# Optimization experiments

Hardware: AMD Instinct MI355X
Metric: run time of the kernel (lower is better)

The kernel has to match this reference:

```python
import jax, jax.numpy as jnp
import numpy as np

VOCAB = 50000
EMB = 128
HID = 256
H = HID // 2          # per-direction LSTM hidden
L = 59                # labelset size
B = 512
S = 256
START, STOP, PAD_LBL = 57, 58, 0
NEG = -10000.0


def setup_inputs() -> dict:
    key = jax.random.key(0)
    ks = jax.random.split(key, 12)
    inp = {}
    inp["x"] = jax.random.randint(ks[0], (B, S), 0, VOCAB)
    inp["y"] = jax.random.randint(ks[1], (B, S), 1, START)  # real labels only
    emb = jax.random.normal(ks[2], (VOCAB, EMB), jnp.float32) * 0.02
    inp["embed"] = emb.at[0].set(0.0)  # padding_idx=0

    def lstm_p(k):
        k1, k2, k3, k4 = jax.random.split(k, 4)
        s = 1.0 / np.sqrt(H)
        return (jax.random.uniform(k1, (4 * H, EMB), jnp.float32, -s, s),
                jax.random.uniform(k2, (4 * H, H), jnp.float32, -s, s),
                jax.random.uniform(k3, (4 * H,), jnp.float32, -s, s),
                jax.random.uniform(k4, (4 * H,), jnp.float32, -s, s))

    inp["Wih_f"], inp["Whh_f"], inp["bih_f"], inp["bhh_f"] = lstm_p(ks[3])
    inp["Wih_b"], inp["Whh_b"], inp["bih_b"], inp["bhh_b"] = lstm_p(ks[4])
    s = 1.0 / np.sqrt(HID)
    inp["Wout"] = jax.random.uniform(ks[5], (L, HID), jnp.float32, -s, s)
    inp["bout"] = jax.random.uniform(ks[6], (L,), jnp.float32, -s, s)
    T = jax.random.normal(ks[7], (L, L), jnp.float32)
    T = T.at[START, :].set(NEG)
    T = T.at[:, STOP].set(NEG)
    T = T.at[START, PAD_LBL].set(NEG)
    T = T.at[STOP + 1:, PAD_LBL].set(NEG)  # no-op here (STOP+1==L), kept for fidelity
    inp["trans"] = T
    inp["h0"] = jax.random.normal(ks[8], (2, B, H), jnp.float32)
    inp["c0"] = jax.random.normal(ks[9], (2, B, H), jnp.float32)
    return inp


def _lstm_scan(emb_seq, Wih, Whh, bih, bhh, h0, c0):
    # emb_seq: (S, B, E); PyTorch gate order i, f, g, o
    def step(carry, x_t):
        h, c = carry
        g = x_t @ Wih.T + bih + h @ Whh.T + bhh          # (B, 4H)
        i, f, gg, o = jnp.split(g, 4, axis=-1)
        c = jax.nn.sigmoid(f) * c + jax.nn.sigmoid(i) * jnp.tanh(gg)
        h = jax.nn.sigmoid(o) * jnp.tanh(c)
        return (h, c), h
    _, hs = jax.lax.scan(step, (h0, c0), emb_seq)
    return hs  # (S, B, H)


def reference(x, y, embed, Wih_f, Whh_f, bih_f, bhh_f,
              Wih_b, Whh_b, bih_b, bhh_b, Wout, bout, trans, h0, c0):
    # ---- BiLSTM emissions ----
    emb = embed[x]                                   # (B, S, E)
    emb = jnp.transpose(emb, (1, 0, 2))              # (S, B, E)
    hf = _lstm_scan(emb, Wih_f, Whh_f, bih_f, bhh_f, h0[0], c0[0])
    hb = _lstm_scan(emb[::-1], Wih_b, Whh_b, bih_b, bhh_b, h0[1], c0[1])[::-1]
    out = jnp.concatenate([hf, hb], axis=-1)         # (S, B, HID)
    feats = jnp.einsum('sbh,lh->bsl', out, Wout) + bout   # (B, S, L)

    # ---- CRF forward algorithm (log-sum-exp scan over time) ----
    alpha0 = jnp.full((B, L), NEG, feats.dtype).at[:, START].set(0.0)
    feats_t = jnp.transpose(feats, (1, 0, 2))        # (S, B, L)

    def fstep(alpha, f_t):
        # alpha_new[b, j] = f_t[b, j] + logsumexp_i(alpha[b, i] + trans[j, i])
        a = jax.nn.logsumexp(alpha[:, None, :] + trans[None, :, :], axis=2)
        return f_t + a, None

    alpha, _ = jax.lax.scan(fstep, alpha0, feats_t)
    fwd_score = jax.nn.logsumexp(alpha + trans[STOP][None, :], axis=1)  # (B,)

    # ---- gold path score ----
    yprev = jnp.concatenate([jnp.full((B, 1), START, y.dtype), y[:, :-1]], axis=1)
    emit = jnp.take_along_axis(feats, y[..., None], axis=2)[..., 0]     # (B, S)
    tr = trans[y, yprev]                                                # (B, S)
    gold = emit.sum(axis=1) + tr.sum(axis=1) + trans[STOP, y[:, -1]]

    return jnp.sum(fwd_score - gold)
```

## Files before the change

### kernel.cpp

```cpp
#include <hip/hip_runtime.h>

#define BB   512
#define SS   256
#define EE   128
#define HH   128
#define LL   59
#define STARTL 57
#define STOPL  58
#define VOCAB 50000

typedef float  f32x4  __attribute__((ext_vector_type(4)));
typedef short  bf16x8 __attribute__((ext_vector_type(8)));
typedef short  s16x4  __attribute__((ext_vector_type(4)));

__device__ __forceinline__ short f2bf(float f) {
    unsigned u = __float_as_uint(f);
    u += 0x7FFFu + ((u >> 16) & 1u);
    return (short)(u >> 16);
}
__device__ __forceinline__ float bf2f(unsigned short s) {
    return __uint_as_float(((unsigned)s) << 16);
}
__device__ __forceinline__ float sigf(float x) {
    float e = __builtin_amdgcn_exp2f(-1.44269504f * x);
    return __builtin_amdgcn_rcpf(1.0f + e);
}
__device__ __forceinline__ float tanhf_(float x) {
    float e = __builtin_amdgcn_exp2f(2.88539008f * x);
    return 1.0f - 2.0f * __builtin_amdgcn_rcpf(e + 1.0f);
}
__device__ __forceinline__ float wmax64(float v) {
    #pragma unroll
    for (int o = 32; o; o >>= 1) v = fmaxf(v, __shfl_xor(v, o));
    return v;
}
__device__ __forceinline__ float wsum64(float v) {
    #pragma unroll
    for (int o = 32; o; o >>= 1) v += __shfl_xor(v, o);
    return v;
}
__device__ __forceinline__ float rlane(float v, int i) {
    return __uint_as_float(__builtin_amdgcn_readlane(__float_as_uint(v), i));
}
__device__ __forceinline__ void bar_lds() {
    asm volatile("s_waitcnt lgkmcnt(0)\n\ts_barrier" ::: "memory");
}

__global__ __launch_bounds__(256) void conv_k(
    const float* __restrict__ embed,
    const float* __restrict__ Wih_f, const float* __restrict__ Wih_b,
    const float* __restrict__ Whh_f, const float* __restrict__ Whh_b,
    const float* __restrict__ bih_f, const float* __restrict__ bhh_f,
    const float* __restrict__ bih_b, const float* __restrict__ bhh_b,
    unsigned short* __restrict__ ebf, unsigned short* __restrict__ wix,
    unsigned short* __restrict__ whb, float* __restrict__ bsum)
{
    const int W1 = VOCAB * EE / 4;
    const int W2 = W1 + 2 * 16384;
    const int W3 = W2 + 2 * 16384;
    const int W4 = W3 + 1024;
    for (int i = blockIdx.x * blockDim.x + threadIdx.x; i < W4;
         i += gridDim.x * blockDim.x) {
        if (i < W1) {
            float4 v = ((const float4*)embed)[i];
            s16x4 s = { f2bf(v.x), f2bf(v.y), f2bf(v.z), f2bf(v.w) };
            ((s16x4*)ebf)[i] = s;
        } else if (i < W2) {
            const int j = i - W1, d = j >> 14, e = j & 16383;
            float4 v = ((const float4*)(d ? Wih_b : Wih_f))[e];
            s16x4 s = { f2bf(v.x), f2bf(v.y), f2bf(v.z), f2bf(v.w) };
            ((s16x4*)wix)[d * 16384 + e] = s;
        } else if (i < W3) {
            const int j = i - W2, d = j >> 14, e = j & 16383;
            float4 v = ((const float4*)(d ? Whh_b : Whh_f))[e];
            s16x4 s = { f2bf(v.x), f2bf(v.y), f2bf(v.z), f2bf(v.w) };
            ((s16x4*)whb)[d * 16384 + e] = s;
        } else {
            const int m = i - W3, d = m >> 9, c = m & 511;
            bsum[d * 512 + c] = d ? (bih_b[c] + bhh_b[c]) : (bih_f[c] + bhh_f[c]);
        }
    }
}

__global__ __launch_bounds__(512, 2) void lstm_f(
    const int* __restrict__ x, const unsigned short* __restrict__ ebf,
    const unsigned short* __restrict__ wix, const unsigned short* __restrict__ whb,
    const float* __restrict__ bsum,
    const float* __restrict__ h0, const float* __restrict__ c0,
    const float* __restrict__ Wout,
    unsigned short* __restrict__ fpF, unsigned short* __restrict__ fpB)
{
    const int tid = threadIdx.x;
    const int w = tid >> 6, l = tid & 63, qd = l >> 4, n = l & 15;
    const int rt = blockIdx.x & 127, dir = blockIdx.x >> 7;
    const int b0 = rt * 4;
    unsigned short* fp = dir ? fpB : fpF;

    __shared__ __align__(16) short hbuf[2][2048];
    __shared__ __align__(16) float gxb[2][4][2048];
    __shared__ int xsh[4 * 256];

    #pragma unroll
    for (int i = 0; i < 2; ++i) ((s16x4*)hbuf)[tid + i * 512] = (s16x4)0;
    #pragma unroll
    for (int i = 0; i < 2; ++i) {
        const int k = tid + i * 512;
        xsh[k] = x[(size_t)(b0 + (k >> 8)) * SS + (k & 255)];
    }

    if (w < 4) {
        const int s0 = 2 * w, s1 = 2 * w + 1;
        bf16x8 fh0[4][4], fh1[4][4];
        #pragma unroll
        for (int g = 0; g < 4; ++g) {
            #pragma unroll
            for (int kk = 0; kk < 4; ++kk) {
                fh0[g][kk] = *(const bf16x8*)(whb + dir * 65536
                             + (size_t)(g * 128 + 16 * s0 + n) * 128 + kk * 32 + qd * 8);
                fh1[g][kk] = *(const bf16x8*)(whb + dir * 65536
                             + (size_t)(g * 128 + 16 * s1 + n) * 128 + kk * 32 + qd * 8);
            }
        }
        bf16x8 wb[4];
        {
            const int col = w * 16 + n;
            #pragma unroll
            for (int kk = 0; kk < 4; ++kk) {
                bf16x8 v = (bf16x8)0;
                if (col < LL) {
                    const float* p = Wout + (size_t)col * 256 + dir * 128 + kk * 32 + qd * 8;
                    #pragma unroll
                    for (int j = 0; j < 8; ++j) v[j] = f2bf(p[j]);
                }
                wb[kk] = v;
            }
        }
        float cst0 = c0[((size_t)dir * BB + b0 + qd) * HH + 16 * s0 + n];
        float cst1 = c0[((size_t)dir * BB + b0 + qd) * HH + 16 * s1 + n];

        __syncthreads();
        {
            const int j = tid >> 7, c = tid & 127;
            hbuf[0][((c >> 3) * 16 + 4 * j) * 8 + (c & 7)] =
                f2bf(h0[((size_t)dir * BB + b0 + j) * HH + c]);
        }
        __syncthreads();

        const int hid0 = 16 * s0 + n, hc0 = hid0 >> 3, ho0 = hid0 & 7;
        const int hid1 = 16 * s1 + n, hc1 = hid1 >> 3, ho1 = hid1 & 7;
        const int gs0 = (s0 * 64 + qd * 16 + n) * 4;
        const int gs1 = (s1 * 64 + qd * 16 + n) * 4;

        f32x4 a0[4], a1[4], pa;
        #pragma unroll
        for (int g = 0; g < 4; ++g) {
            a0[g] = (f32x4){0.f, 0.f, 0.f, 0.f};
            a1[g] = (f32x4){0.f, 0.f, 0.f, 0.f};
        }
        pa = (f32x4){0.f, 0.f, 0.f, 0.f};

        unsigned short* fpp = fp + ((size_t)(b0 + qd) * SS + (dir ? SS - 1 : 0)) * 64
                            + w * 16 + n;
        const ptrdiff_t fpd = dir ? -64 : 64;

        for (int ts = 0; ts < SS; ++ts) {
            const int cur = ts & 1, nxt = cur ^ 1;
            const int gbuf = (ts >> 2) & 1, tau = ts & 3;

            const f32x4 g0 = *(const f32x4*)&gxb[gbuf][tau][gs0];
            const f32x4 g1 = *(const f32x4*)&gxb[gbuf][tau][gs1];

            bf16x8 ah[4];
            #pragma unroll
            for (int kk = 0; kk < 4; ++kk)
                ah[kk] = *(const bf16x8*)&hbuf[cur][((kk * 4 + qd) * 16 + n) * 8];

            a0[0][0] = g0[0]; a0[1][0] = g0[1]; a0[2][0] = g0[2]; a0[3][0] = g0[3];
            a1[0][0] = g1[0]; a1[1][0] = g1[1]; a1[2][0] = g1[2]; a1[3][0] = g1[3];

            #pragma unroll
            for (int kk = 0; kk < 4; ++kk) {
                #pragma unroll
                for (int g = 0; g < 4; ++g) {
                    a0[g] = __builtin_amdgcn_mfma_f32_16x16x32_bf16(ah[kk], fh0[g][kk], a0[g], 0, 0, 0);
                    a1[g] = __builtin_amdgcn_mfma_f32_16x16x32_bf16(ah[kk], fh1[g][kk], a1[g], 0, 0, 0);
                }
            }

            if (ts > 0) {
                pa[0] = 0.f;
                #pragma unroll
                for (int kk = 0; kk < 4; ++kk)
                    pa = __builtin_amdgcn_mfma_f32_16x16x32_bf16(ah[kk], wb[kk], pa, 0, 0, 0);
                *fpp = (unsigned short)f2bf(pa[0]);
                fpp += fpd;
            }

            {
                const float iv0 = sigf(a0[0][0]), fv0 = sigf(a0[1][0]);
                const float gv0 = tanhf_(a0[2][0]), ov0 = sigf(a0[3][0]);
                const float cc0 = fv0 * cst0 + iv0 * gv0;
                cst0 = cc0;
                hbuf[nxt][(hc0 * 16 + 4 * qd) * 8 + ho0] = f2bf(ov0 * tanhf_(cc0));
                const float iv1 = sigf(a1[0][0]), fv1 = sigf(a1[1][0]);
                const float gv1 = tanhf_(a1[2][0]), ov1 = sigf(a1[3][0]);
                const float cc1 = fv1 * cst1 + iv1 * gv1;
                cst1 = cc1;
                hbuf[nxt][(hc1 * 16 + 4 * qd) * 8 + ho1] = f2bf(ov1 * tanhf_(cc1));
            }
            bar_lds();
        }

        {
            pa[0] = 0.f;
            #pragma unroll
            for (int kk = 0; kk < 4; ++kk) {
                const bf16x8 a = *(const bf16x8*)&hbuf[0][((kk * 4 + qd) * 16 + n) * 8];
                pa = __builtin_amdgcn_mfma_f32_16x16x32_bf16(a, wb[kk], pa, 0, 0, 0);
            }
            *fpp = (unsigned short)f2bf(pa[0]);
        }
    } else {
        const int s0 = 2 * (w - 4), s1 = s0 + 1;
        bf16x8 fx0[4][4], fx1[4][4]; float bs0[4], bs1[4];
        #pragma unroll
        for (int g = 0; g < 4; ++g) {
            bs0[g] = bsum[dir * 512 + g * 128 + 16 * s0 + n];
            bs1[g] = bsum[dir * 512 + g * 128 + 16 * s1 + n];
            #pragma unroll
            for (int kk = 0; kk < 4; ++kk) {
                fx0[g][kk] = *(const bf16x8*)(wix + dir * 65536
                             + (size_t)(g * 128 + 16 * s0 + n) * 128 + kk * 32 + qd * 8);
                fx1[g][kk] = *(const bf16x8*)(wix + dir * 65536
                             + (size_t)(g * 128 + 16 * s1 + n) * 128 + kk * 32 + qd * 8);
            }
        }
        const int gs0 = (s0 * 64 + qd * 16 + n) * 4;
        const int gs1 = (s1 * 64 + qd * 16 + n) * 4;
        const int jb   = n >> 2;
        const int tau  = n & 3;
        const int jrow = jb * 256;

        auto loadfrag = [&](int G, bf16x8* e) {
            const int t  = 4 * G + tau;
            const int te = dir ? (SS - 1 - t) : t;
            const int xi = xsh[jrow + te];
            const unsigned short* er = ebf + (size_t)xi * EE + qd * 8;
            e[0] = *(const bf16x8*)(er);
            e[1] = *(const bf16x8*)(er + 32);
            e[2] = *(const bf16x8*)(er + 64);
            e[3] = *(const bf16x8*)(er + 96);
        };
        auto computeS = [&](const bf16x8* e, const bf16x8 (*fx)[4],
                            const float* bs, int gsv, int buf) {
            f32x4 c[4] = { {0,0,0,0}, {0,0,0,0}, {0,0,0,0}, {0,0,0,0} };
            #pragma unroll
            for (int g = 0; g < 4; ++g) {
                #pragma unroll
                for (int kk = 0; kk < 4; ++kk)
                    c[g] = __builtin_amdgcn_mfma_f32_16x16x32_bf16(e[kk], fx[g][kk], c[g], 0, 0, 0);
            }
            #pragma unroll
            for (int r = 0; r < 4; ++r) {
                f32x4 p = { c[0][r] + bs[0], c[1][r] + bs[1],
                            c[2][r] + bs[2], c[3][r] + bs[3] };
                *(f32x4*)&gxb[buf][r][gsv] = p;
            }
        };

        __syncthreads();
        bf16x8 eA[4], eB[4];
        loadfrag(0, eA);
        computeS(eA, fx0, bs0, gs0, 0);
        computeS(eA, fx1, bs1, gs1, 0);
        loadfrag(1, eB);
        __syncthreads();

        auto xgroup = [&](int G, bf16x8* use, bf16x8* pre) {
            if (G + 2 < SS / 4) loadfrag(G + 2, pre);
            if (G + 1 < SS / 4) computeS(use, fx0, bs0, gs0, (G + 1) & 1);
            bar_lds();
            if (G + 1 < SS / 4) computeS(use, fx1, bs1, gs1, (G + 1) & 1);
            bar_lds();
            bar_lds();
            bar_lds();
        };
        for (int G = 0; G < SS / 4; G += 2) {
            xgroup(G,     eB, eA);
            xgroup(G + 1, eA, eB);
        }
    }
}

__global__ __launch_bounds__(64, 1) void crf_k(
    const unsigned short* __restrict__ fpF, const unsigned short* __restrict__ fpB,
    const float* __restrict__ bout, const int* __restrict__ y,
    const float* __restrict__ trans, float* __restrict__ out)
{
    const int j = threadIdx.x;
    const int b = blockIdx.x;
    const size_t bS = (size_t)b * SS;
    const bool valid = (j < LL);
    const int  jr = valid ? j : (LL - 1);
    const float L2E = 1.44269504f, LN2 = 0.69314718f;

    float etr[LL];
    #pragma unroll
    for (int i = 0; i < LL; ++i) {
        const float t = trans[jr * LL + i];
        etr[i] = valid ? __builtin_amdgcn_exp2f(t * L2E) : 0.0f;
    }
    const float bo = valid ? bout[jr] : 0.0f;

    float alpha = valid ? ((j == STARTL) ? 0.0f : -10000.0f * L2E) : -1e30f;
    float Kn = 0.0f;

    float fF[8], fB[8];
    #pragma unroll
    for (int q = 0; q < 8; ++q) {
        fF[q] = bf2f(fpF[(bS + q) * 64 + j]);
        fB[q] = bf2f(fpB[(bS + q) * 64 + j]);
    }

    for (int t0 = 0; t0 < SS; t0 += 8) {
        float nF[8], nB[8];
        #pragma unroll
        for (int q = 0; q < 8; ++q) { nF[q] = 0.0f; nB[q] = 0.0f; }
        if (t0 + 8 < SS) {
            #pragma unroll
            for (int q = 0; q < 8; ++q) {
                nF[q] = bf2f(fpF[(bS + t0 + 8 + q) * 64 + j]);
                nB[q] = bf2f(fpB[(bS + t0 + 8 + q) * 64 + j]);
            }
        }
        float fs[8];
        #pragma unroll
        for (int q = 0; q < 8; ++q) fs[q] = (fF[q] + fB[q] + bo) * L2E;

        #pragma unroll
        for (int u = 0; u < 8; ++u) {
            const float Kc = Kn;
            const float ea = __builtin_amdgcn_exp2f(alpha - Kc);
            Kn = fmaxf(rlane(alpha, 1), rlane(alpha, STARTL));
            float d0 = 0.f, d1 = 0.f, d2 = 0.f, d3 = 0.f;
            float d4 = 0.f, d5 = 0.f, d6 = 0.f, d7 = 0.f;
            #pragma unroll
            for (int i = 0; i < 56; i += 8) {
                d0 += etr[i]     * rlane(ea, i);
                d1 += etr[i + 1] * rlane(ea, i + 1);
                d2 += etr[i + 2] * rlane(ea, i + 2);
                d3 += etr[i + 3] * rlane(ea, i + 3);
                d4 += etr[i + 4] * rlane(ea, i + 4);
                d5 += etr[i + 5] * rlane(ea, i + 5);
                d6 += etr[i + 6] * rlane(ea, i + 6);
                d7 += etr[i + 7] * rlane(ea, i + 7);
            }
            d0 += etr[56] * rlane(ea, 56);
            d1 += etr[57] * rlane(ea, 57);
            d2 += etr[58] * rlane(ea, 58);
            const float dot = ((d0 + d1) + (d2 + d3)) + ((d4 + d5) + (d6 + d7));
            alpha = fs[u] + Kc + __builtin_amdgcn_logf(dot);
        }
        #pragma unroll
        for (int q = 0; q < 8; ++q) { fF[q] = nF[q]; fB[q] = nB[q]; }
    }

    const float v  = alpha * LN2 + trans[STOPL * LL + jr];
    const float m2 = wmax64(v);
    const float s  = wsum64(__builtin_amdgcn_exp2f((v - m2) * L2E));
    const float fwd = m2 + LN2 * __builtin_amdgcn_logf(s);

    float g = 0.0f;
    #pragma unroll
    for (int q = 0; q < 4; ++q) {
        const int t  = q * 64 + j;
        const int yt = y[bS + t];
        const int yp = t ? y[bS + t - 1] : STARTL;
        g += bf2f(fpF[(bS + t) * 64 + yt]) + bf2f(fpB[(bS + t) * 64 + yt])
           + bout[yt] + trans[yt * LL + yp];
    }
    g = wsum64(g);

    if (j == 0) {
        g += trans[STOPL * LL + y[bS + SS - 1]];
        atomicAdd(out, fwd - g);
    }
}

extern "C" void kernel_launch(void* const* d_in, const int* in_sizes, int n_in,
                              void* d_out, int out_size, void* d_ws, size_t ws_size,
                              hipStream_t stream)
{
    (void)in_sizes; (void)n_in; (void)out_size; (void)ws_size;
    const int*   x      = (const int*)  d_in[0];
    const int*   y      = (const int*)  d_in[1];
    const float* embed  = (const float*)d_in[2];
    const float* Wih_f  = (const float*)d_in[3];
    const float* Whh_f  = (const float*)d_in[4];
    const float* bih_f  = (const float*)d_in[5];
    const float* bhh_f  = (const float*)d_in[6];
    const float* Wih_b  = (const float*)d_in[7];
    const float* Whh_b  = (const float*)d_in[8];
    const float* bih_b  = (const float*)d_in[9];
    const float* bhh_b  = (const float*)d_in[10];
    const float* Wout   = (const float*)d_in[11];
    const float* bout   = (const float*)d_in[12];
    const float* trans  = (const float*)d_in[13];
    const float* h0     = (const float*)d_in[14];
    const float* c0     = (const float*)d_in[15];

    const size_t MiB = 1ull << 20;
    unsigned short* fpF  = (unsigned short*)d_ws;
    unsigned short* fpB  = (unsigned short*)((char*)d_ws + 16 * MiB);
    unsigned short* ebf  = (unsigned short*)((char*)d_ws + 32 * MiB);
    unsigned short* wix  = (unsigned short*)((char*)d_ws + 45 * MiB);
    unsigned short* whb  = (unsigned short*)((char*)d_ws + 45 * MiB + 256 * 1024);
    float*          bsum = (float*)((char*)d_ws + 45 * MiB + 512 * 1024);

    hipMemsetAsync(d_out, 0, sizeof(float), stream);
    conv_k<<<2048, 256, 0, stream>>>(embed, Wih_f, Wih_b, Whh_f, Whh_b,
                                     bih_f, bhh_f, bih_b, bhh_b,
                                     ebf, wix, whb, bsum);
    lstm_f<<<256, 512, 0, stream>>>(x, ebf, wix, whb, bsum, h0, c0, Wout,
                                    fpF, fpB);
    crf_k<<<BB, 64, 0, stream>>>(fpF, fpB, bout, y, trans, (float*)d_out);
}
```

Measured before the change: 373.2 us.

## Split CRF forward recursion into meet-in-the-middle forward and backward waves

The CRF kernel now runs two waves per batch row. One runs the forward alpha recursion over the first half of the sequence, and the other runs a backward beta recursion from STOP over the second half using the transposed transitions. The two halves are combined through LDS to form the partition function. This halves the serial dependency chain of the log-sum-exp scan, at the cost of doubling threads per block and adding a sync and LDS exchange. The gold-score computation moves to the backward wave so it overlaps with the combine step.

```diff
diff --git a/kernel.cpp b/kernel.cpp
--- a/kernel.cpp
+++ b/kernel.cpp
@@ -292,45 +292,56 @@
     }
 }
 
-__global__ __launch_bounds__(64, 1) void crf_k(
+__global__ __launch_bounds__(128, 1) void crf_k(
     const unsigned short* __restrict__ fpF, const unsigned short* __restrict__ fpB,
     const float* __restrict__ bout, const int* __restrict__ y,
     const float* __restrict__ trans, float* __restrict__ out)
 {
-    const int j = threadIdx.x;
+    const int tid = threadIdx.x;
+    const int wv = tid >> 6;
+    const int j = tid & 63;
     const int b = blockIdx.x;
     const size_t bS = (size_t)b * SS;
     const bool valid = (j < LL);
     const int  jr = valid ? j : (LL - 1);
     const float L2E = 1.44269504f, LN2 = 0.69314718f;
 
+    __shared__ float exch[64];
+    __shared__ float gshare;
+
     float etr[LL];
     #pragma unroll
     for (int i = 0; i < LL; ++i) {
-        const float t = trans[jr * LL + i];
+        const float t = wv ? trans[i * LL + jr] : trans[jr * LL + i];
         etr[i] = valid ? __builtin_amdgcn_exp2f(t * L2E) : 0.0f;
     }
     const float bo = valid ? bout[jr] : 0.0f;
 
-    float alpha = valid ? ((j == STARTL) ? 0.0f : -10000.0f * L2E) : -1e30f;
+    float st;
+    if (wv == 0) st = valid ? ((j == STARTL) ? 0.0f : -10000.0f * L2E) : -1e30f;
+    else         st = valid ? trans[STOPL * LL + jr] * L2E : -1e30f;
     float Kn = 0.0f;
 
+    auto tAt = [&](int u) { return wv ? (SS - 1 - u) : u; };
+
     float fF[8], fB[8];
     #pragma unroll
     for (int q = 0; q < 8; ++q) {
-        fF[q] = bf2f(fpF[(bS + q) * 64 + j]);
-        fB[q] = bf2f(fpB[(bS + q) * 64 + j]);
-    }
-
-    for (int t0 = 0; t0 < SS; t0 += 8) {
+        const int t = tAt(q);
+        fF[q] = bf2f(fpF[(bS + t) * 64 + j]);
+        fB[q] = bf2f(fpB[(bS + t) * 64 + j]);
+    }
+
+    for (int u0 = 0; u0 < SS / 2; u0 += 8) {
         float nF[8], nB[8];
         #pragma unroll
         for (int q = 0; q < 8; ++q) { nF[q] = 0.0f; nB[q] = 0.0f; }
-        if (t0 + 8 < SS) {
+        if (u0 + 8 < SS / 2) {
             #pragma unroll
             for (int q = 0; q < 8; ++q) {
-                nF[q] = bf2f(fpF[(bS + t0 + 8 + q) * 64 + j]);
-                nB[q] = bf2f(fpB[(bS + t0 + 8 + q) * 64 + j]);
+                const int t = tAt(u0 + 8 + q);
+                nF[q] = bf2f(fpF[(bS + t) * 64 + j]);
+                nB[q] = bf2f(fpB[(bS + t) * 64 + j]);
             }
         }
         float fs[8];
@@ -339,51 +350,81 @@
 
         #pragma unroll
         for (int u = 0; u < 8; ++u) {
-            const float Kc = Kn;
-            const float ea = __builtin_amdgcn_exp2f(alpha - Kc);
-            Kn = fmaxf(rlane(alpha, 1), rlane(alpha, STARTL));
-            float d0 = 0.f, d1 = 0.f, d2 = 0.f, d3 = 0.f;
-            float d4 = 0.f, d5 = 0.f, d6 = 0.f, d7 = 0.f;
-            #pragma unroll
-            for (int i = 0; i < 56; i += 8) {
-                d0 += etr[i]     * rlane(ea, i);
-                d1 += etr[i + 1] * rlane(ea, i + 1);
-                d2 += etr[i + 2] * rlane(ea, i + 2);
-                d3 += etr[i + 3] * rlane(ea, i + 3);
-                d4 += etr[i + 4] * rlane(ea, i + 4);
-                d5 += etr[i + 5] * rlane(ea, i + 5);
-                d6 += etr[i + 6] * rlane(ea, i + 6);
-                d7 += etr[i + 7] * rlane(ea, i + 7);
-            }
-            d0 += etr[56] * rlane(ea, 56);
-            d1 += etr[57] * rlane(ea, 57);
-            d2 += etr[58] * rlane(ea, 58);
-            const float dot = ((d0 + d1) + (d2 + d3)) + ((d4 + d5) + (d6 + d7));
-            alpha = fs[u] + Kc + __builtin_amdgcn_logf(dot);
+            if (wv == 0) {
+                const float Kc = Kn;
+                const float ea = __builtin_amdgcn_exp2f(st - Kc);
+                Kn = fmaxf(rlane(st, 1), rlane(st, STARTL));
+                float d0 = 0.f, d1 = 0.f, d2 = 0.f, d3 = 0.f;
+                float d4 = 0.f, d5 = 0.f, d6 = 0.f, d7 = 0.f;
+                #pragma unroll
+                for (int i = 0; i < 56; i += 8) {
+                    d0 += etr[i]     * rlane(ea, i);
+                    d1 += etr[i + 1] * rlane(ea, i + 1);
+                    d2 += etr[i + 2] * rlane(ea, i + 2);
+                    d3 += etr[i + 3] * rlane(ea, i + 3);
+                    d4 += etr[i + 4] * rlane(ea, i + 4);
+                    d5 += etr[i + 5] * rlane(ea, i + 5);
+                    d6 += etr[i + 6] * rlane(ea, i + 6);
+                    d7 += etr[i + 7] * rlane(ea, i + 7);
+                }
+                d0 += etr[56] * rlane(ea, 56);
+                d1 += etr[57] * rlane(ea, 57);
+                d2 += etr[58] * rlane(ea, 58);
+                const float dot = ((d0 + d1) + (d2 + d3)) + ((d4 + d5) + (d6 + d7));
+                st = fs[u] + Kc + __builtin_amdgcn_logf(dot);
+            } else {
+                const float g = fs[u] + st;
+                const float Kc = Kn;
+                const float eg = __builtin_amdgcn_exp2f(g - Kc);
+                Kn = rlane(g, 1);
+                float d0 = 0.f, d1 = 0.f, d2 = 0.f, d3 = 0.f;
+                float d4 = 0.f, d5 = 0.f, d6 = 0.f, d7 = 0.f;
+                #pragma unroll
+                for (int i = 0; i < 56; i += 8) {
+                    d0 += etr[i]     * rlane(eg, i);
+                    d1 += etr[i + 1] * rlane(eg, i + 1);
+                    d2 += etr[i + 2] * rlane(eg, i + 2);
+                    d3 += etr[i + 3] * rlane(eg, i + 3);
+                    d4 += etr[i + 4] * rlane(eg, i + 4);
+                    d5 += etr[i + 5] * rlane(eg, i + 5);
+                    d6 += etr[i + 6] * rlane(eg, i + 6);
+                    d7 += etr[i + 7] * rlane(eg, i + 7);
+                }
+                d0 += etr[56] * rlane(eg, 56);
+                d1 += etr[57] * rlane(eg, 57);
+                d2 += etr[58] * rlane(eg, 58);
+                const float dot = ((d0 + d1) + (d2 + d3)) + ((d4 + d5) + (d6 + d7));
+                st = Kc + __builtin_amdgcn_logf(dot);
+            }
         }
         #pragma unroll
         for (int q = 0; q < 8; ++q) { fF[q] = nF[q]; fB[q] = nB[q]; }
     }
 
-    const float v  = alpha * LN2 + trans[STOPL * LL + jr];
-    const float m2 = wmax64(v);
-    const float s  = wsum64(__builtin_amdgcn_exp2f((v - m2) * L2E));
-    const float fwd = m2 + LN2 * __builtin_amdgcn_logf(s);
-
-    float g = 0.0f;
-    #pragma unroll
-    for (int q = 0; q < 4; ++q) {
-        const int t  = q * 64 + j;
-        const int yt = y[bS + t];
-        const int yp = t ? y[bS + t - 1] : STARTL;
-        g += bf2f(fpF[(bS + t) * 64 + yt]) + bf2f(fpB[(bS + t) * 64 + yt])
-           + bout[yt] + trans[yt * LL + yp];
-    }
-    g = wsum64(g);
-
-    if (j == 0) {
-        g += trans[STOPL * LL + y[bS + SS - 1]];
-        atomicAdd(out, fwd - g);
+    if (wv == 1) {
+        float g = 0.0f;
+        #pragma unroll
+        for (int q = 0; q < 4; ++q) {
+            const int t  = q * 64 + j;
+            const int yt = y[bS + t];
+            const int yp = t ? y[bS + t - 1] : STARTL;
+            g += bf2f(fpF[(bS + t) * 64 + yt]) + bf2f(fpB[(bS + t) * 64 + yt])
+               + bout[yt] + trans[yt * LL + yp];
+        }
+        g = wsum64(g);
+        if (j == 0) {
+            g += trans[STOPL * LL + y[bS + SS - 1]];
+            gshare = g;
+        }
+        exch[j] = st;
+    }
+    __syncthreads();
+    if (wv == 0) {
+        const float v2 = valid ? (st + exch[j]) : -1e30f;
+        const float m2 = wmax64(v2);
+        const float s  = wsum64(__builtin_amdgcn_exp2f(v2 - m2));
+        const float fwd = LN2 * (m2 + __builtin_amdgcn_logf(s));
+        if (j == 0) atomicAdd(out, fwd - gshare);
     }
 }
 
@@ -423,5 +464,5 @@
                                      ebf, wix, whb, bsum);
     lstm_f<<<256, 512, 0, stream>>>(x, ebf, wix, whb, bsum, h0, c0, Wout,
                                     fpF, fpB);
-    crf_k<<<BB, 64, 0, stream>>>(fpF, fpB, bout, y, trans, (float*)d_out);
-}
+    crf_k<<<BB, 128, 0, stream>>>(fpF, fpB, bout, y, trans, (float*)d_out);
+}
```

Result: faster. 342.8 us (-8.1%).
